# Performance work log

Measured on AMD Instinct MI355X. Metric: run time of the kernel, lower is better.

## Reference

```python
import jax, jax.numpy as jnp
import numpy as np

N, H, L, O = 8192, 512, 3, 512
LN_EPS = 1e-5


def setup_inputs() -> dict:
    key = jax.random.key(0)
    ks = jax.random.split(key, 8)
    # sparse symmetric adjacency with positive weights, zero diagonal
    u = jax.random.uniform(ks[0], (N, N))
    w = jax.random.uniform(ks[1], (N, N)) * 0.9 + 0.1
    A = jnp.where(u < 0.004, w, 0.0)
    A = (A + A.T) * 0.5
    A = A * (1.0 - jnp.eye(N, dtype=A.dtype))
    s = 0.02
    return {
        "node_feat": jax.random.normal(ks[2], (1, N, H), jnp.float32),
        "adj": A[None],
        "conv_w": jax.random.normal(ks[3], (L, H, H), jnp.float32) * s,
        "conv_b": jnp.zeros((L, H), jnp.float32),
        "mlp_w": jax.random.normal(ks[4], (L, H, H), jnp.float32) * s,
        "mlp_b": jnp.zeros((L, H), jnp.float32),
        "ln_g": jnp.ones((L, H), jnp.float32),
        "ln_b": jnp.zeros((L, H), jnp.float32),
        "lin_w": jax.random.normal(ks[5], (H, O), jnp.float32) * s,
        "lin_b": jnp.zeros((O,), jnp.float32),
    }


def _layer_norm(x, g, b):
    mu = jnp.mean(x, axis=-1, keepdims=True)
    var = jnp.mean(jnp.square(x - mu), axis=-1, keepdims=True)
    return (x - mu) * jax.lax.rsqrt(var + LN_EPS) * g + b


def reference(node_feat, adj, conv_w, conv_b, mlp_w, mlp_b, ln_g, ln_b, lin_w, lin_b):
    x = node_feat[0]          # [N, H]
    A = adj[0]                # [N, N]
    A = jnp.where(A > 0, A, 0.0)  # edges are positive entries only
    # gcn_norm: add self-loops (weight 1) only where missing
    d = jnp.diagonal(A)
    A1 = A + jnp.diag(jnp.where(d > 0, 0.0, 1.0))
    # deg scattered at target (edge_index[1] = column)
    deg = jnp.sum(A1, axis=0)
    dinv = jnp.where(deg > 0, deg ** -0.5, 0.0)
    Ahat = dinv[:, None] * A1 * dinv[None, :]  # [N, N]
    for l in range(L):
        # GCNConv: linear, propagate (aggregate at col), bias
        x = Ahat.T @ (x @ conv_w[l]) + conv_b[l]
        # MLP: Linear -> LayerNorm -> ReLU
        x = jax.nn.relu(_layer_norm(x @ mlp_w[l] + mlp_b[l], ln_g[l], ln_b[l]))
    mu = (x @ lin_w + lin_b)[None]  # [1, N, O]
    return mu
```

## Files before the change

kernel.cpp:

```cpp
#include <hip/hip_runtime.h>

#define NN 8192
#define HD 512
#define NL 3
#define CAPQ 48
#define CAPR (4 * CAPQ)
#define NWB (273 * NL)
#define LN_EPS 1e-5f

typedef _Float16 f16;
typedef _Float16 f16x8 __attribute__((ext_vector_type(8)));
typedef _Float16 f16x4 __attribute__((ext_vector_type(4)));
typedef _Float16 f16x2 __attribute__((ext_vector_type(2)));
typedef float f32x4 __attribute__((ext_vector_type(4)));

__device__ __forceinline__ unsigned short f16_bits(f16 h) {
  union { f16 h; unsigned short u; } x; x.h = h; return x.u;
}
__device__ __forceinline__ f16 bits_f16(unsigned short u) {
  union { unsigned short u; f16 h; } x; x.u = u; return x.h;
}

__global__ __launch_bounds__(256) void k_prep(const float* __restrict__ A,
                                              const float* __restrict__ convw,
                                              const float* __restrict__ mlpw,
                                              const float* __restrict__ convb,
                                              const float* __restrict__ mlpb,
                                              const float* __restrict__ lw,
                                              unsigned* __restrict__ ell,
                                              int* __restrict__ nnz8q,
                                              float* __restrict__ psum,
                                              f16* __restrict__ WlT,
                                              float* __restrict__ bl,
                                              f16* __restrict__ lwT) {
  const int b = blockIdx.x;
  const int t = threadIdx.x;

  if (b < NWB) {
    const int l = b / 273;
    const int bx = b % 273;
    if (bx < 256) {
      const int m0 = bx * 2;
      const float* Wc = convw + (size_t)l * HD * HD;
      const float* Wm = mlpw + (size_t)l * HD * HD;
      f16* o = WlT + (size_t)l * HD * HD;
      float a00 = 0.f, a01 = 0.f, a10 = 0.f, a11 = 0.f;
      const float* wc0 = Wc + (size_t)m0 * HD;
      const float* wc1 = Wc + (size_t)(m0 + 1) * HD;
      for (int k = 0; k < HD; k++) {
        const float w0 = Wm[(size_t)k * HD + t];
        const float w1 = Wm[(size_t)k * HD + t + 256];
        const float c0 = wc0[k];
        const float c1 = wc1[k];
        a00 = fmaf(c0, w0, a00);
        a01 = fmaf(c0, w1, a01);
        a10 = fmaf(c1, w0, a10);
        a11 = fmaf(c1, w1, a11);
      }
      o[(size_t)t * HD + m0] = (f16)a00;
      o[(size_t)(t + 256) * HD + m0] = (f16)a01;
      o[(size_t)t * HD + m0 + 1] = (f16)a10;
      o[(size_t)(t + 256) * HD + m0 + 1] = (f16)a11;
    } else if (bx == 256) {
      const float* Wm = mlpw + (size_t)l * HD * HD;
      float acc0 = mlpb[l * HD + t];
      float acc1 = mlpb[l * HD + t + 256];
      for (int k = 0; k < HD; k++) {
        const float cb = convb[l * HD + k];
        acc0 = fmaf(cb, Wm[(size_t)k * HD + t], acc0);
        acc1 = fmaf(cb, Wm[(size_t)k * HD + t + 256], acc1);
      }
      bl[l * HD + t] = acc0;
      bl[l * HD + t + 256] = acc1;
    } else if (l == 0) {
      const int base = (bx - 257) * 16384;
      #pragma unroll 4
      for (int j = 0; j < 64; j++) {
        const int idx = base + j * 256 + t;
        const int k = idx >> 9, n = idx & 511;
        lwT[(size_t)n * HD + k] = (f16)lw[idx];
      }
    }
    return;
  }

  __shared__ int wtot[4];
  __shared__ float wsum[4];
  const int sb = b - NWB;
  const int r = sb >> 2;
  const int seg = sb & 3;
  const int lane = t & 63;
  const int wv = t >> 6;
  const float4* aseg = (const float4*)(A + (size_t)r * NN + seg * 2048);
  unsigned* er = ell + (size_t)r * CAPR + seg * CAPQ;

  const float4 v0 = aseg[t];
  const float4 v1 = aseg[t + 256];
  int c = (v0.x > 0.f) + (v0.y > 0.f) + (v0.z > 0.f) + (v0.w > 0.f) +
          (v1.x > 0.f) + (v1.y > 0.f) + (v1.z > 0.f) + (v1.w > 0.f);
  float s = v0.x + v0.y + v0.z + v0.w + v1.x + v1.y + v1.z + v1.w;

  int inc = c;
  #pragma unroll
  for (int d = 1; d < 64; d <<= 1) {
    int vv = __shfl_up(inc, d);
    if (lane >= d) inc += vv;
  }
  float ss = s;
  #pragma unroll
  for (int m = 1; m < 64; m <<= 1) ss += __shfl_xor(ss, m);
  if (lane == 63) wtot[wv] = inc;
  if (lane == 0) wsum[wv] = ss;
  __syncthreads();
  int base = inc - c;
  for (int w = 0; w < wv; w++) base += wtot[w];

  int o = base;
  const int cb0 = seg * 2048 + t * 4;
  const int cb1 = seg * 2048 + (t + 256) * 4;
  {
    float vals[4] = {v0.x, v0.y, v0.z, v0.w};
    #pragma unroll
    for (int q = 0; q < 4; q++) {
      if (vals[q] > 0.f) {
        if (o < CAPQ) er[o] = ((unsigned)f16_bits((f16)vals[q]) << 16) | (unsigned)(cb0 + q);
        o++;
      }
    }
  }
  {
    float vals[4] = {v1.x, v1.y, v1.z, v1.w};
    #pragma unroll
    for (int q = 0; q < 4; q++) {
      if (vals[q] > 0.f) {
        if (o < CAPQ) er[o] = ((unsigned)f16_bits((f16)vals[q]) << 16) | (unsigned)(cb1 + q);
        o++;
      }
    }
  }
  if (t == 255) {
    int ne = wtot[0] + wtot[1] + wtot[2] + wtot[3];
    if (ne > CAPQ) ne = CAPQ;
    const bool own = (seg == (r >> 11));
    if (own && ne < CAPQ) { er[ne] = (0x3C00u << 16) | (unsigned)r; ne++; }
    const int n8 = (ne + 7) & ~7;
    for (int k = ne; k < n8; k++) er[k] = (unsigned)r;
    nnz8q[r * 4 + seg] = n8;
    psum[r * 4 + seg] = wsum[0] + wsum[1] + wsum[2] + wsum[3];
  }
}

__global__ __launch_bounds__(256) void k_deg(const float* __restrict__ psum,
                                             const float* __restrict__ x0,
                                             float* __restrict__ dinv,
                                             f16* __restrict__ xs) {
  const int r = blockIdx.x * 4 + (threadIdx.x >> 6);
  const int lane = threadIdx.x & 63;
  const float4 ps = *(const float4*)(psum + (size_t)r * 4);
  const float di = rsqrtf(ps.x + ps.y + ps.z + ps.w + 1.f);
  if (lane == 0) dinv[r] = di;
  const float4* xr = (const float4*)(x0 + (size_t)r * HD);
  const float4 a = xr[lane * 2];
  const float4 bq = xr[lane * 2 + 1];
  f16x8 o = {(f16)(a.x * di), (f16)(a.y * di), (f16)(a.z * di), (f16)(a.w * di),
             (f16)(bq.x * di), (f16)(bq.y * di), (f16)(bq.z * di), (f16)(bq.w * di)};
  *(f16x8*)(xs + (size_t)r * HD + lane * 8) = o;
}

__global__ __launch_bounds__(256) void k_spmm(const unsigned* __restrict__ ell,
                                              const int* __restrict__ nnz8q,
                                              const float* __restrict__ dinv,
                                              const f16* __restrict__ xs,
                                              f16* __restrict__ y) {
  const int bid = blockIdx.x;
  const int chunk = bid & 3;
  const int rb = bid >> 2;
  const int r = __builtin_amdgcn_readfirstlane(rb * 4 + (threadIdx.x >> 6));
  const int lane = threadIdx.x & 63;
  const int c0 = chunk * 128 + lane * 2;
  const unsigned* erow = ell + (size_t)r * CAPR;
  const int4 nn = *(const int4*)(nnz8q + (size_t)r * 4);
  const int ne8s[4] = {nn.x >> 3, nn.y >> 3, nn.z >> 3, nn.w >> 3};
  const f16* xc = xs + c0;
  float a0 = 0.f, a1 = 0.f;
  #pragma unroll
  for (int seg = 0; seg < 4; seg++) {
    const uint4* er = (const uint4*)(erow + seg * CAPQ);
    const int ne8 = ne8s[seg];
    for (int e8 = 0; e8 < ne8; e8++) {
      const uint4 ea = er[e8 * 2];
      const uint4 eb = er[e8 * 2 + 1];
      unsigned wv[8] = {ea.x, ea.y, ea.z, ea.w, eb.x, eb.y, eb.z, eb.w};
      f16x2 xv[8];
      #pragma unroll
      for (int q = 0; q < 8; q++)
        xv[q] = *(const f16x2*)(xc + (size_t)(wv[q] & 0xFFFFu) * HD);
      #pragma unroll
      for (int q = 0; q < 8; q++) {
        const float fw = (float)bits_f16((unsigned short)(wv[q] >> 16));
        a0 = fmaf(fw, (float)xv[q][0], a0);
        a1 = fmaf(fw, (float)xv[q][1], a1);
      }
    }
  }
  const float s = dinv[r];
  f16x2 o = {(f16)(a0 * s), (f16)(a1 * s)};
  *(f16x2*)(y + (size_t)r * HD + c0) = o;
}

__global__ __launch_bounds__(512) void k_gemm_ln(const f16* __restrict__ y,
                                                 const f16* __restrict__ WT,
                                                 const float* __restrict__ bias,
                                                 const float* __restrict__ g,
                                                 const float* __restrict__ bb,
                                                 const float* __restrict__ dscale,
                                                 f16* __restrict__ outp) {
  __shared__ float red[32][4][2];
  const int t = threadIdx.x;
  const int lane = t & 63;
  const int w = t >> 6;
  const int wm = w >> 2;
  const int wn = w & 3;
  const int m0 = blockIdx.x * 32;
  const int rl = lane & 15, kg = (lane >> 4) * 8;
  const f16* aP = y + (size_t)(m0 + wm * 16 + rl) * HD + kg;
  const f16* bP = WT + (size_t)(wn * 128 + rl) * HD + kg;

  f32x4 acc[8];
  #pragma unroll
  for (int j = 0; j < 8; j++) { f32x4 z = {0.f, 0.f, 0.f, 0.f}; acc[j] = z; }

  #pragma unroll 2
  for (int ks = 0; ks < HD; ks += 32) {
    const f16x8 af = *(const f16x8*)(aP + ks);
    #pragma unroll
    for (int j = 0; j < 8; j++) {
      const f16x8 bf = *(const f16x8*)(bP + (size_t)j * 16 * HD + ks);
      acc[j] = __builtin_amdgcn_mfma_f32_16x16x32_f16(af, bf, acc[j], 0, 0, 0);
    }
  }

  const int cg = lane >> 4, cl = lane & 15;
  float av[8][4];
  #pragma unroll
  for (int j = 0; j < 8; j++) {
    const float bv = bias[wn * 128 + j * 16 + cl];
    #pragma unroll
    for (int r = 0; r < 4; r++) av[j][r] = acc[j][r] + bv;
  }
  #pragma unroll
  for (int r = 0; r < 4; r++) {
    float s = 0.f, sq = 0.f;
    #pragma unroll
    for (int j = 0; j < 8; j++) { s += av[j][r]; sq += av[j][r] * av[j][r]; }
    #pragma unroll
    for (int m = 1; m < 16; m <<= 1) { s += __shfl_xor(s, m); sq += __shfl_xor(sq, m); }
    if (cl == 0) {
      red[wm * 16 + cg * 4 + r][wn][0] = s;
      red[wm * 16 + cg * 4 + r][wn][1] = sq;
    }
  }
  __syncthreads();
  #pragma unroll
  for (int r = 0; r < 4; r++) {
    const int rb = wm * 16 + cg * 4 + r;
    float s = 0.f, sq = 0.f;
    #pragma unroll
    for (int q = 0; q < 4; q++) { s += red[rb][q][0]; sq += red[rb][q][1]; }
    const float mu = s * (1.f / HD);
    const float rs = rsqrtf(sq * (1.f / HD) - mu * mu + LN_EPS);
    const int row = m0 + rb;
    const float dsc = dscale ? dscale[row] : 1.f;
    #pragma unroll
    for (int j = 0; j < 8; j++) {
      const int col = wn * 128 + j * 16 + cl;
      const float val = fmaxf((av[j][r] - mu) * rs * g[col] + bb[col], 0.f) * dsc;
      outp[(size_t)row * HD + col] = (f16)val;
    }
  }
}

__global__ __launch_bounds__(256) void k_gemm_direct(const f16* __restrict__ A,
                                                     const f16* __restrict__ BT,
                                                     float* __restrict__ C,
                                                     const float* __restrict__ bias) {
  const int t = threadIdx.x;
  const int lane = t & 63;
  const int wave = t >> 6;
  const int wm = wave >> 1, wn = wave & 1;
  const int m0 = blockIdx.x * 128, n0 = blockIdx.y * 128;
  const int rl = lane & 15, kg = (lane >> 4) * 8;

  const f16* aP[4];
  const f16* bP[4];
  #pragma unroll
  for (int i = 0; i < 4; i++)
    aP[i] = A + (size_t)(m0 + wm * 64 + i * 16 + rl) * HD + kg;
  #pragma unroll
  for (int j = 0; j < 4; j++)
    bP[j] = BT + (size_t)(n0 + wn * 64 + j * 16 + rl) * HD + kg;

  f32x4 acc[4][4];
  #pragma unroll
  for (int i = 0; i < 4; i++)
    #pragma unroll
    for (int j = 0; j < 4; j++) {
      f32x4 z = {0.f, 0.f, 0.f, 0.f};
      acc[i][j] = z;
    }

  #pragma unroll 4
  for (int ks = 0; ks < HD; ks += 32) {
    f16x8 af[4], bf[4];
    #pragma unroll
    for (int i = 0; i < 4; i++) af[i] = *(const f16x8*)(aP[i] + ks);
    #pragma unroll
    for (int j = 0; j < 4; j++) bf[j] = *(const f16x8*)(bP[j] + ks);
    #pragma unroll
    for (int i = 0; i < 4; i++)
      #pragma unroll
      for (int j = 0; j < 4; j++)
        acc[i][j] = __builtin_amdgcn_mfma_f32_16x16x32_f16(af[i], bf[j], acc[i][j], 0, 0, 0);
  }

  const int cg = lane >> 4, cl = lane & 15;
  #pragma unroll
  for (int i = 0; i < 4; i++) {
    #pragma unroll
    for (int j = 0; j < 4; j++) {
      const int col = n0 + wn * 64 + j * 16 + cl;
      const float bv = bias ? bias[col] : 0.f;
      #pragma unroll
      for (int rr = 0; rr < 4; rr++) {
        const int row = m0 + wm * 64 + i * 16 + cg * 4 + rr;
        C[(size_t)row * HD + col] = acc[i][j][rr] + bv;
      }
    }
  }
}

extern "C" void kernel_launch(void* const* d_in, const int* in_sizes, int n_in,
                              void* d_out, int out_size, void* d_ws, size_t ws_size,
                              hipStream_t stream) {
  const float* node_feat = (const float*)d_in[0];
  const float* adj       = (const float*)d_in[1];
  const float* conv_w    = (const float*)d_in[2];
  const float* conv_b    = (const float*)d_in[3];
  const float* mlp_w     = (const float*)d_in[4];
  const float* mlp_b     = (const float*)d_in[5];
  const float* ln_g      = (const float*)d_in[6];
  const float* ln_b      = (const float*)d_in[7];
  const float* lin_w     = (const float*)d_in[8];
  const float* lin_b     = (const float*)d_in[9];
  float* out = (float*)d_out;

  char* p = (char*)d_ws;
  unsigned* ell = (unsigned*)p; p += (size_t)NN * CAPR * 4;
  int* nnz8q = (int*)p;  p += (size_t)NN * 4 * 4;
  float* psum = (float*)p; p += (size_t)NN * 4 * 4;
  float* dinv = (float*)p; p += (size_t)NN * 4;
  f16* xsA   = (f16*)p;   p += (size_t)NN * HD * 2;
  f16* xsB   = (f16*)p;   p += (size_t)NN * HD * 2;
  f16* ybuf  = (f16*)p;   p += (size_t)NN * HD * 2;
  f16* WlT   = (f16*)p;   p += (size_t)NL * HD * HD * 2;
  f16* lwT   = (f16*)p;   p += (size_t)HD * HD * 2;
  float* bl  = (float*)p; p += (size_t)NL * HD * 4;

  k_prep<<<NWB + 4 * NN, 256, 0, stream>>>(adj, conv_w, mlp_w, conv_b, mlp_b,
                                           lin_w, ell, nnz8q, psum, WlT, bl, lwT);
  k_deg<<<NN / 4, 256, 0, stream>>>(psum, node_feat, dinv, xsA);

  f16* xcur = xsA;
  for (int l = 0; l < NL; l++) {
    k_spmm<<<NN, 256, 0, stream>>>(ell, nnz8q, dinv, xcur, ybuf);
    f16* nxt = (xcur == xsA) ? xsB : xsA;
    k_gemm_ln<<<NN / 32, 512, 0, stream>>>(ybuf, WlT + (size_t)l * HD * HD,
                                           bl + l * HD, ln_g + l * HD, ln_b + l * HD,
                                           (l < 2) ? dinv : nullptr, nxt);
    xcur = nxt;
  }
  k_gemm_direct<<<dim3(64, 4), 256, 0, stream>>>(xcur, lwT, out, lin_b);
}
```

Measured before the change: 329.3 us.

## Process adjacency segments per wavefront with persistent blocks and double-buffered loads

The adjacency compaction now runs on a fixed grid of 2048 blocks. Each wavefront handles four row-segments instead of each 256-thread block handling one. Loads of the next segment are issued into a second register buffer before the current one is processed, which overlaps the HBM reads with compaction. It also removes the block-level shared-memory scan and __syncthreads in favour of wave-only shuffles. The cost is higher register use per thread from holding 16 float4 values, which may reduce occupancy and the number of loads in flight.

```diff
diff --git a/kernel.cpp b/kernel.cpp
--- a/kernel.cpp
+++ b/kernel.cpp
@@ -6,6 +6,7 @@
 #define CAPQ 48
 #define CAPR (4 * CAPQ)
 #define NWB (273 * NL)
+#define NSB 2048
 #define LN_EPS 1e-5f
 
 typedef _Float16 f16;
@@ -84,70 +85,69 @@
     return;
   }
 
-  __shared__ int wtot[4];
-  __shared__ float wsum[4];
-  const int sb = b - NWB;
-  const int r = sb >> 2;
-  const int seg = sb & 3;
   const int lane = t & 63;
-  const int wv = t >> 6;
-  const float4* aseg = (const float4*)(A + (size_t)r * NN + seg * 2048);
-  unsigned* er = ell + (size_t)r * CAPR + seg * CAPQ;
-
-  const float4 v0 = aseg[t];
-  const float4 v1 = aseg[t + 256];
-  int c = (v0.x > 0.f) + (v0.y > 0.f) + (v0.z > 0.f) + (v0.w > 0.f) +
-          (v1.x > 0.f) + (v1.y > 0.f) + (v1.z > 0.f) + (v1.w > 0.f);
-  float s = v0.x + v0.y + v0.z + v0.w + v1.x + v1.y + v1.z + v1.w;
-
-  int inc = c;
-  #pragma unroll
-  for (int d = 1; d < 64; d <<= 1) {
-    int vv = __shfl_up(inc, d);
-    if (lane >= d) inc += vv;
-  }
-  float ss = s;
-  #pragma unroll
-  for (int m = 1; m < 64; m <<= 1) ss += __shfl_xor(ss, m);
-  if (lane == 63) wtot[wv] = inc;
-  if (lane == 0) wsum[wv] = ss;
-  __syncthreads();
-  int base = inc - c;
-  for (int w = 0; w < wv; w++) base += wtot[w];
-
-  int o = base;
-  const int cb0 = seg * 2048 + t * 4;
-  const int cb1 = seg * 2048 + (t + 256) * 4;
-  {
-    float vals[4] = {v0.x, v0.y, v0.z, v0.w};
-    #pragma unroll
-    for (int q = 0; q < 4; q++) {
-      if (vals[q] > 0.f) {
-        if (o < CAPQ) er[o] = ((unsigned)f16_bits((f16)vals[q]) << 16) | (unsigned)(cb0 + q);
-        o++;
-      }
-    }
-  }
-  {
-    float vals[4] = {v1.x, v1.y, v1.z, v1.w};
-    #pragma unroll
-    for (int q = 0; q < 4; q++) {
-      if (vals[q] > 0.f) {
-        if (o < CAPQ) er[o] = ((unsigned)f16_bits((f16)vals[q]) << 16) | (unsigned)(cb1 + q);
-        o++;
-      }
-    }
-  }
-  if (t == 255) {
-    int ne = wtot[0] + wtot[1] + wtot[2] + wtot[3];
-    if (ne > CAPQ) ne = CAPQ;
-    const bool own = (seg == (r >> 11));
-    if (own && ne < CAPQ) { er[ne] = (0x3C00u << 16) | (unsigned)r; ne++; }
-    const int n8 = (ne + 7) & ~7;
-    for (int k = ne; k < n8; k++) er[k] = (unsigned)r;
-    nnz8q[r * 4 + seg] = n8;
-    psum[r * 4 + seg] = wsum[0] + wsum[1] + wsum[2] + wsum[3];
-  }
+  const int wid = (b - NWB) * 4 + (t >> 6);
+
+  auto LOADQ = [&](int qidx, float4* v) {
+    const int r = qidx >> 2, seg = qidx & 3;
+    const float4* aseg = (const float4*)(A + (size_t)r * NN + seg * 2048);
+    #pragma unroll
+    for (int i = 0; i < 8; i++) v[i] = aseg[lane + i * 64];
+  };
+
+  auto PROC = [&](int qidx, const float4* v) {
+    const int r = qidx >> 2, seg = qidx & 3;
+    unsigned* er = ell + (size_t)qidx * CAPQ;
+    int c = 0;
+    float s = 0.f;
+    #pragma unroll
+    for (int i = 0; i < 8; i++) {
+      c += (v[i].x > 0.f) + (v[i].y > 0.f) + (v[i].z > 0.f) + (v[i].w > 0.f);
+      s += v[i].x + v[i].y + v[i].z + v[i].w;
+    }
+    int inc = c;
+    #pragma unroll
+    for (int d = 1; d < 64; d <<= 1) {
+      int vv = __shfl_up(inc, d);
+      if (lane >= d) inc += vv;
+    }
+    float ss = s;
+    #pragma unroll
+    for (int m = 1; m < 64; m <<= 1) ss += __shfl_xor(ss, m);
+    int o = inc - c;
+    #pragma unroll
+    for (int i = 0; i < 8; i++) {
+      const int cb = seg * 2048 + (lane + i * 64) * 4;
+      float vals[4] = {v[i].x, v[i].y, v[i].z, v[i].w};
+      #pragma unroll
+      for (int q = 0; q < 4; q++) {
+        if (vals[q] > 0.f) {
+          if (o < CAPQ) er[o] = ((unsigned)f16_bits((f16)vals[q]) << 16) | (unsigned)(cb + q);
+          o++;
+        }
+      }
+    }
+    int ne = __shfl(inc, 63);
+    if (lane == 0) {
+      if (ne > CAPQ) ne = CAPQ;
+      const bool own = (seg == (r >> 11));
+      if (own && ne < CAPQ) { er[ne] = (0x3C00u << 16) | (unsigned)r; ne++; }
+      const int n8 = (ne + 7) & ~7;
+      for (int k = ne; k < n8; k++) er[k] = (unsigned)r;
+      nnz8q[qidx] = n8;
+      psum[qidx] = ss;
+    }
+  };
+
+  float4 va[8], vb[8];
+  LOADQ(wid, va);
+  LOADQ(wid + 8192, vb);
+  PROC(wid, va);
+  LOADQ(wid + 16384, va);
+  PROC(wid + 8192, vb);
+  LOADQ(wid + 24576, vb);
+  PROC(wid + 16384, va);
+  PROC(wid + 24576, vb);
 }
 
 __global__ __launch_bounds__(256) void k_deg(const float* __restrict__ psum,
@@ -366,8 +366,8 @@
   f16* lwT   = (f16*)p;   p += (size_t)HD * HD * 2;
   float* bl  = (float*)p; p += (size_t)NL * HD * 4;
 
-  k_prep<<<NWB + 4 * NN, 256, 0, stream>>>(adj, conv_w, mlp_w, conv_b, mlp_b,
-                                           lin_w, ell, nnz8q, psum, WlT, bl, lwT);
+  k_prep<<<NWB + NSB, 256, 0, stream>>>(adj, conv_w, mlp_w, conv_b, mlp_b,
+                                        lin_w, ell, nnz8q, psum, WlT, bl, lwT);
   k_deg<<<NN / 4, 256, 0, stream>>>(psum, node_feat, dinv, xsA);
 
   f16* xcur = xsA;
```

New measurement: 330.7 us. About the same (+0.4%).
